# Performance work log

Hardware: AMD Instinct MI355X
Metric: run time of the kernel (lower is better)

The kernel has to match this reference:

```python
import jax, jax.numpy as jnp
import numpy as np

N, C_IN, C_OUT, H = 4096, 1024, 512, 4
D = C_OUT // H  # per-head output dim
TEMP = 1.0


def setup_inputs() -> dict:
    key = jax.random.key(0)
    ks = jax.random.split(key, 6)
    node_feats = jax.random.normal(ks[0], (N, C_IN), dtype=jnp.float32)
    # sparse 0/1 adjacency mask, avg degree ~ 0.02*N
    adj_matrix = jax.random.bernoulli(ks[1], 0.02, (N, N)).astype(jnp.float32)
    lim_w = np.sqrt(6.0 / (C_IN + D))
    lim_v = np.sqrt(6.0 / (D + 1))
    W = jax.random.uniform(ks[2], (H, C_IN, D), jnp.float32, -lim_w, lim_w)
    b = jnp.zeros((H, D), dtype=jnp.float32)
    v0 = jax.random.uniform(ks[3], (H, D), jnp.float32, -lim_v, lim_v)
    v1 = jax.random.uniform(ks[4], (H, D), jnp.float32, -lim_v, lim_v)
    return {"node_feats": node_feats, "adj_matrix": adj_matrix,
            "W": W, "b": b, "v0": v0, "v1": v1}


def reference(node_feats, adj_matrix, W, b, v0, v1):
    # per-head linear projection: [H, N, D]
    h = jnp.einsum('nc,hcd->hnd', node_feats, W) + b[:, None, :]
    f1 = jnp.einsum('hnd,hd->hn', h, v0)  # [H, N]
    f2 = jnp.einsum('hnd,hd->hn', h, v1)  # [H, N]
    logits = adj_matrix[None, :, :] * (f1[:, :, None] + f2[:, None, :])
    # torch to_sparse drops exact zeros; sparse.softmax normalizes over
    # the remaining (nonzero) entries only, zeros stay zero when densified.
    mask = logits != 0
    vals = (jax.nn.sigmoid(logits) - 0.5) / TEMP
    rowmax = jnp.max(jnp.where(mask, vals, -1e30), axis=-1, keepdims=True)
    e = jnp.where(mask, jnp.exp(vals - rowmax), 0.0)
    denom = jnp.sum(e, axis=-1, keepdims=True)
    p = jnp.where(denom > 0, e / jnp.maximum(denom, 1e-30), 0.0)
    out = jnp.einsum('hnm,hmd->hnd', p, h)  # [H, N, D]
    # concat heads along feature dim -> [N, H*D]
    return out.transpose(1, 0, 2).reshape(node_feats.shape[0], -1)
```

## Files before the change

### kernel.cpp

```cpp
#include <hip/hip_runtime.h>
#include <hip/hip_bf16.h>

#define N_NODES 4096
#define C_IN    1024
#define H_HEADS 4
#define D_HEAD  128
#define C_OUT   512
#define DEG_CAP 256

typedef __attribute__((ext_vector_type(8))) short short8;
typedef __attribute__((ext_vector_type(8))) unsigned short u16x8;
typedef __attribute__((ext_vector_type(4))) float f32x4;

__device__ __forceinline__ unsigned short f2bf(float f) {
    unsigned u = __float_as_uint(f);
    u += 0x7FFFu + ((u >> 16) & 1u);
    return (unsigned short)(u >> 16);
}
__device__ __forceinline__ float bf2f(unsigned short u) {
    return __uint_as_float((unsigned)u << 16);
}
__device__ __forceinline__ float sigv(float s) {
    return 1.f / (1.f + __expf(-s)) - 0.5f;
}

#define GLOAD_LDS16(gp, lp)                                                        \
    __builtin_amdgcn_global_load_lds(                                              \
        (const __attribute__((address_space(1))) unsigned int*)(gp),               \
        (__attribute__((address_space(3))) unsigned int*)(lp), 16, 0, 0)

__global__ void k_cvt(const float* __restrict__ X, const float* __restrict__ W,
                      unsigned short* __restrict__ Xb, unsigned short* __restrict__ Wt,
                      float* __restrict__ F12) {
    if (blockIdx.x < 2048) {
        int g = blockIdx.x * blockDim.x + threadIdx.x;
        const float4* s = (const float4*)(X + (size_t)g * 8);
        float4 a = s[0], b = s[1];
        ushort4 p0, p1;
        p0.x = f2bf(a.x); p0.y = f2bf(a.y); p0.z = f2bf(a.z); p0.w = f2bf(a.w);
        p1.x = f2bf(b.x); p1.y = f2bf(b.y); p1.z = f2bf(b.z); p1.w = f2bf(b.w);
        ushort4* d = (ushort4*)(Xb + (size_t)g * 8);
        d[0] = p0; d[1] = p1;
    } else if (blockIdx.x < 2560) {
        int g = (blockIdx.x - 2048) * blockDim.x + threadIdx.x;
        int o = g * 4;
        int c  = o & 1023;
        int hd = o >> 10;
        int d  = hd & 127;
        int h  = hd >> 7;
        const float* src = W + (size_t)h * C_IN * D_HEAD + (size_t)c * D_HEAD + d;
        ushort4 p;
        p.x = f2bf(src[0 * D_HEAD]);
        p.y = f2bf(src[1 * D_HEAD]);
        p.z = f2bf(src[2 * D_HEAD]);
        p.w = f2bf(src[3 * D_HEAD]);
        *(ushort4*)(Wt + o) = p;
    } else {
        int g = (blockIdx.x - 2560) * blockDim.x + threadIdx.x;
        *(f32x4*)(F12 + (size_t)g * 4) = (f32x4){0.f, 0.f, 0.f, 0.f};
    }
}

__global__ void k_gemm(const unsigned short* __restrict__ Xb,
                       const unsigned short* __restrict__ Wt,
                       const float* __restrict__ bias,
                       const float* __restrict__ v0, const float* __restrict__ v1,
                       unsigned short* __restrict__ Hb,
                       float* __restrict__ F1, float* __restrict__ F2) {
    __shared__ __align__(16) unsigned short ldsA[2 * 64 * 64];
    __shared__ __align__(16) unsigned short ldsB[2 * 64 * 64];
    const int t    = threadIdx.x;
    const int lane = t & 63;
    const int wid  = t >> 6;
    const int wrow = wid >> 1, wcol = wid & 1;
    const int bid  = blockIdx.x;
    const int lin  = (bid & 7) * 64 + (bid >> 3);
    const int rowStart = (lin >> 3) * 64;
    const int colStart = (lin & 7) * 64;

    f32x4 acc[2][2];
#pragma unroll
    for (int m = 0; m < 2; ++m)
#pragma unroll
        for (int n = 0; n < 2; ++n) acc[m][n] = (f32x4){0.f, 0.f, 0.f, 0.f};

    const int lrow = lane >> 2;
    const int lkq  = (lane & 3) ^ ((lane >> 3) & 3);

    auto stage = [&](int buf, int k0) {
#pragma unroll
        for (int ii = 0; ii < 2; ++ii) {
            int c  = wid * 2 + ii;
            int h  = c >> 2, rb = c & 3;
            const unsigned short* g =
                Xb + (size_t)(rowStart + rb * 16 + lrow) * C_IN + k0 + h * 32 + lkq * 8;
            GLOAD_LDS16(g, ldsA + buf * 4096 + h * 2048 + rb * 512);
        }
#pragma unroll
        for (int ii = 0; ii < 2; ++ii) {
            int c  = wid * 2 + ii;
            int h  = c >> 2, db = c & 3;
            const unsigned short* g =
                Wt + (size_t)(colStart + db * 16 + lrow) * C_IN + k0 + h * 32 + lkq * 8;
            GLOAD_LDS16(g, ldsB + buf * 4096 + h * 2048 + db * 512);
        }
    };

    stage(0, 0);
    __syncthreads();

    const int fr = lane & 15;
    const int sw = ((lane >> 4) ^ ((fr >> 1) & 3)) * 8;
    int cur = 0;
    for (int kt = 0; kt < 16; ++kt) {
        if (kt < 15) stage(cur ^ 1, (kt + 1) * 64);
        const unsigned short* __restrict__ lA = ldsA + cur * 4096;
        const unsigned short* __restrict__ lB = ldsB + cur * 4096;
#pragma unroll
        for (int h = 0; h < 2; ++h) {
            short8 bfr[2];
#pragma unroll
            for (int n = 0; n < 2; ++n)
                bfr[n] = *(const short8*)(lB + h * 2048 + (wcol * 32 + n * 16 + fr) * 32 + sw);
#pragma unroll
            for (int m = 0; m < 2; ++m) {
                short8 a = *(const short8*)(lA + h * 2048 + (wrow * 32 + m * 16 + fr) * 32 + sw);
#pragma unroll
                for (int n = 0; n < 2; ++n)
                    acc[m][n] = __builtin_amdgcn_mfma_f32_16x16x32_bf16(a, bfr[n], acc[m][n], 0, 0, 0);
            }
        }
        __syncthreads();
        cur ^= 1;
    }

    const int c0 = colStart + wcol * 32 + (lane & 15);
    const int c1 = c0 + 16;
    const int head = c0 >> 7;
    const float bb0 = bias[c0], bb1 = bias[c1];
    const float v0c0 = v0[c0], v0c1 = v0[c1];
    const float v1c0 = v1[c0], v1c1 = v1[c1];
#pragma unroll
    for (int m = 0; m < 2; ++m) {
        int row_g = rowStart + wrow * 32 + m * 16 + (lane >> 4) * 4;
#pragma unroll
        for (int r = 0; r < 4; ++r) {
            float h0 = acc[m][0][r] + bb0;
            float h1 = acc[m][1][r] + bb1;
            Hb[(size_t)(row_g + r) * C_OUT + c0] = f2bf(h0);
            Hb[(size_t)(row_g + r) * C_OUT + c1] = f2bf(h1);
            float p1 = h0 * v0c0 + h1 * v0c1;
            float p2 = h0 * v1c0 + h1 * v1c1;
#pragma unroll
            for (int off = 8; off; off >>= 1) {
                p1 += __shfl_xor(p1, off);
                p2 += __shfl_xor(p2, off);
            }
            if ((lane & 15) == 0) {
                atomicAdd(&F1[(row_g + r) * 4 + head], p1);
                atomicAdd(&F2[(row_g + r) * 4 + head], p2);
            }
        }
    }
}

__global__ void k_attn2(const float* __restrict__ adj, const unsigned short* __restrict__ Hb,
                        const float* __restrict__ F1, const float* __restrict__ F2,
                        float* __restrict__ Out) {
    __shared__ unsigned short jl[DEG_CAP];
    __shared__ float ev[DEG_CAP * 4];
    __shared__ float partial[4][C_OUT];
    __shared__ float dred[4][4];
    __shared__ int   wtot[4];

    const int i    = blockIdx.x;
    const int t    = threadIdx.x;
    const int lane = t & 63;
    const int wid  = t >> 6;
    const int headl = lane >> 4;

    const float4* arow = (const float4*)(adj + (size_t)i * N_NODES);
    float4 av[4];
#pragma unroll
    for (int r = 0; r < 4; ++r) av[r] = arow[r * 256 + t];
    float4 f1v = *(const float4*)(F1 + i * 4);

    int cnt = 0;
#pragma unroll
    for (int r = 0; r < 4; ++r)
        cnt += (av[r].x != 0.f) + (av[r].y != 0.f) + (av[r].z != 0.f) + (av[r].w != 0.f);
    int v = cnt;
#pragma unroll
    for (int off = 1; off < 64; off <<= 1) {
        int u = __shfl_up(v, off);
        if (lane >= off) v += u;
    }
    if (lane == 63) wtot[wid] = v;
    __syncthreads();
    int wpre = 0, total = 0;
#pragma unroll
    for (int w = 0; w < 4; ++w) {
        int tw = wtot[w];
        if (w < wid) wpre += tw;
        total += tw;
    }
    const int nv = min(total, DEG_CAP);
    int off = wpre + v - cnt;
#pragma unroll
    for (int r = 0; r < 4; ++r) {
        int j0 = (r * 256 + t) * 4;
        if (av[r].x != 0.f) { if (off < DEG_CAP) jl[off] = (unsigned short)j0;       off++; }
        if (av[r].y != 0.f) { if (off < DEG_CAP) jl[off] = (unsigned short)(j0 + 1); off++; }
        if (av[r].z != 0.f) { if (off < DEG_CAP) jl[off] = (unsigned short)(j0 + 2); off++; }
        if (av[r].w != 0.f) { if (off < DEG_CAP) jl[off] = (unsigned short)(j0 + 3); off++; }
    }
    __syncthreads();

    float e0 = 0.f, e1 = 0.f, e2 = 0.f, e3 = 0.f;
    if (t < nv) {
        int j = jl[t];
        float4 f2v = *(const float4*)(F2 + j * 4);
        float s0 = f1v.x + f2v.x, s1 = f1v.y + f2v.y;
        float s2 = f1v.z + f2v.z, s3 = f1v.w + f2v.w;
        e0 = (s0 != 0.f) ? __expf(sigv(s0)) : 0.f;
        e1 = (s1 != 0.f) ? __expf(sigv(s1)) : 0.f;
        e2 = (s2 != 0.f) ? __expf(sigv(s2)) : 0.f;
        e3 = (s3 != 0.f) ? __expf(sigv(s3)) : 0.f;
        ev[t * 4 + 0] = e0; ev[t * 4 + 1] = e1;
        ev[t * 4 + 2] = e2; ev[t * 4 + 3] = e3;
    }
#pragma unroll
    for (int o2 = 32; o2; o2 >>= 1) {
        e0 += __shfl_xor(e0, o2); e1 += __shfl_xor(e1, o2);
        e2 += __shfl_xor(e2, o2); e3 += __shfl_xor(e3, o2);
    }
    if (lane == 0) {
        dred[wid][0] = e0; dred[wid][1] = e1; dred[wid][2] = e2; dred[wid][3] = e3;
    }
    __syncthreads();

    float acc0[8], acc1[8];
#pragma unroll
    for (int k = 0; k < 8; ++k) { acc0[k] = 0.f; acc1[k] = 0.f; }
    const unsigned short* __restrict__ hp = Hb + lane * 8;

    int jj = wid;
#pragma unroll 4
    for (; jj + 4 < nv; jj += 8) {
        int ja = jl[jj], jb = jl[jj + 4];
        float ea = ev[jj * 4 + headl];
        float eb = ev[(jj + 4) * 4 + headl];
        u16x8 ha = *(const u16x8*)(hp + (size_t)ja * C_OUT);
        u16x8 hb = *(const u16x8*)(hp + (size_t)jb * C_OUT);
#pragma unroll
        for (int k = 0; k < 8; ++k) acc0[k] += ea * bf2f(ha[k]);
#pragma unroll
        for (int k = 0; k < 8; ++k) acc1[k] += eb * bf2f(hb[k]);
    }
    if (jj < nv) {
        int ja = jl[jj];
        float ea = ev[jj * 4 + headl];
        u16x8 ha = *(const u16x8*)(hp + (size_t)ja * C_OUT);
#pragma unroll
        for (int k = 0; k < 8; ++k) acc0[k] += ea * bf2f(ha[k]);
    }

    f32x4 lo = {acc0[0] + acc1[0], acc0[1] + acc1[1], acc0[2] + acc1[2], acc0[3] + acc1[3]};
    f32x4 hi = {acc0[4] + acc1[4], acc0[5] + acc1[5], acc0[6] + acc1[6], acc0[7] + acc1[7]};
    *(f32x4*)&partial[wid][lane * 8]     = lo;
    *(f32x4*)&partial[wid][lane * 8 + 4] = hi;
    __syncthreads();

    int head = t >> 6;
    float dn = dred[0][head] + dred[1][head] + dred[2][head] + dred[3][head];
    int c = 2 * t;
    float s0 = partial[0][c] + partial[1][c] + partial[2][c] + partial[3][c];
    float s1 = partial[0][c + 1] + partial[1][c + 1] + partial[2][c + 1] + partial[3][c + 1];
    float2 o;
    if (dn > 0.f) {
        float inv = 1.f / fmaxf(dn, 1e-30f);
        o.x = s0 * inv;
        o.y = s1 * inv;
    } else {
        o.x = 0.f; o.y = 0.f;
    }
    *(float2*)(Out + (size_t)i * C_OUT + c) = o;
}

extern "C" void kernel_launch(void* const* d_in, const int* in_sizes, int n_in,
                              void* d_out, int out_size, void* d_ws, size_t ws_size,
                              hipStream_t stream) {
    const float* X   = (const float*)d_in[0];
    const float* adj = (const float*)d_in[1];
    const float* W   = (const float*)d_in[2];
    const float* b   = (const float*)d_in[3];
    const float* v0  = (const float*)d_in[4];
    const float* v1  = (const float*)d_in[5];
    float* out = (float*)d_out;

    char* ws = (char*)d_ws;
    unsigned short* Wt  = (unsigned short*)ws;
    unsigned short* Xb  = (unsigned short*)(ws + (size_t)1 * 1024 * 1024);
    unsigned short* Hb  = (unsigned short*)(ws + (size_t)9 * 1024 * 1024);
    float*          F1  = (float*)(ws + (size_t)13 * 1024 * 1024);
    float*          F2  = F1 + N_NODES * 4;

    k_cvt<<<2592, 256, 0, stream>>>(X, W, Xb, Wt, F1);
    k_gemm<<<512, 256, 0, stream>>>(Xb, Wt, b, v0, v1, Hb, F1, F2);
    k_attn2<<<N_NODES, 256, 0, stream>>>(adj, Hb, F1, F2, out);
}
```

Measured before the change: 66.06 us.

## Overlap adjacency compaction with projection GEMM in a merged launch

Moves the dense adjacency scan and neighbor-index compaction out of the attention kernel into extra blocks of the GEMM launch, writing per-row index lists and counts to workspace. The 64MB adjacency read can then run concurrently with the MFMA projection, while the PV kernel reads only compact indices. The cost is an extra global round trip for the index lists and a merged kernel that uses 32KB of LDS for every block, including the scan blocks.

```diff
diff --git a/kernel.cpp b/kernel.cpp
--- a/kernel.cpp
+++ b/kernel.cpp
@@ -61,117 +61,160 @@
     }
 }
 
-__global__ void k_gemm(const unsigned short* __restrict__ Xb,
+__global__ void k_work(const unsigned short* __restrict__ Xb,
                        const unsigned short* __restrict__ Wt,
                        const float* __restrict__ bias,
                        const float* __restrict__ v0, const float* __restrict__ v1,
+                       const float* __restrict__ adj,
                        unsigned short* __restrict__ Hb,
-                       float* __restrict__ F1, float* __restrict__ F2) {
-    __shared__ __align__(16) unsigned short ldsA[2 * 64 * 64];
-    __shared__ __align__(16) unsigned short ldsB[2 * 64 * 64];
+                       float* __restrict__ F1, float* __restrict__ F2,
+                       unsigned short* __restrict__ idx, int* __restrict__ nnz) {
+    __shared__ __align__(16) unsigned char smem[32768];
     const int t    = threadIdx.x;
     const int lane = t & 63;
     const int wid  = t >> 6;
-    const int wrow = wid >> 1, wcol = wid & 1;
-    const int bid  = blockIdx.x;
-    const int lin  = (bid & 7) * 64 + (bid >> 3);
-    const int rowStart = (lin >> 3) * 64;
-    const int colStart = (lin & 7) * 64;
-
-    f32x4 acc[2][2];
-#pragma unroll
-    for (int m = 0; m < 2; ++m)
-#pragma unroll
-        for (int n = 0; n < 2; ++n) acc[m][n] = (f32x4){0.f, 0.f, 0.f, 0.f};
-
-    const int lrow = lane >> 2;
-    const int lkq  = (lane & 3) ^ ((lane >> 3) & 3);
-
-    auto stage = [&](int buf, int k0) {
-#pragma unroll
-        for (int ii = 0; ii < 2; ++ii) {
-            int c  = wid * 2 + ii;
-            int h  = c >> 2, rb = c & 3;
-            const unsigned short* g =
-                Xb + (size_t)(rowStart + rb * 16 + lrow) * C_IN + k0 + h * 32 + lkq * 8;
-            GLOAD_LDS16(g, ldsA + buf * 4096 + h * 2048 + rb * 512);
-        }
-#pragma unroll
-        for (int ii = 0; ii < 2; ++ii) {
-            int c  = wid * 2 + ii;
-            int h  = c >> 2, db = c & 3;
-            const unsigned short* g =
-                Wt + (size_t)(colStart + db * 16 + lrow) * C_IN + k0 + h * 32 + lkq * 8;
-            GLOAD_LDS16(g, ldsB + buf * 4096 + h * 2048 + db * 512);
-        }
-    };
-
-    stage(0, 0);
-    __syncthreads();
-
-    const int fr = lane & 15;
-    const int sw = ((lane >> 4) ^ ((fr >> 1) & 3)) * 8;
-    int cur = 0;
-    for (int kt = 0; kt < 16; ++kt) {
-        if (kt < 15) stage(cur ^ 1, (kt + 1) * 64);
-        const unsigned short* __restrict__ lA = ldsA + cur * 4096;
-        const unsigned short* __restrict__ lB = ldsB + cur * 4096;
-#pragma unroll
-        for (int h = 0; h < 2; ++h) {
-            short8 bfr[2];
-#pragma unroll
-            for (int n = 0; n < 2; ++n)
-                bfr[n] = *(const short8*)(lB + h * 2048 + (wcol * 32 + n * 16 + fr) * 32 + sw);
-#pragma unroll
-            for (int m = 0; m < 2; ++m) {
-                short8 a = *(const short8*)(lA + h * 2048 + (wrow * 32 + m * 16 + fr) * 32 + sw);
+
+    if (blockIdx.x < 512) {
+        unsigned short* ldsA = (unsigned short*)smem;
+        unsigned short* ldsB = ldsA + 2 * 64 * 64;
+        const int wrow = wid >> 1, wcol = wid & 1;
+        const int bid  = blockIdx.x;
+        const int lin  = (bid & 7) * 64 + (bid >> 3);
+        const int rowStart = (lin >> 3) * 64;
+        const int colStart = (lin & 7) * 64;
+
+        f32x4 acc[2][2];
+#pragma unroll
+        for (int m = 0; m < 2; ++m)
+#pragma unroll
+            for (int n = 0; n < 2; ++n) acc[m][n] = (f32x4){0.f, 0.f, 0.f, 0.f};
+
+        const int lrow = lane >> 2;
+        const int lkq  = (lane & 3) ^ ((lane >> 3) & 3);
+
+        auto stage = [&](int buf, int k0) {
+#pragma unroll
+            for (int ii = 0; ii < 2; ++ii) {
+                int c  = wid * 2 + ii;
+                int h  = c >> 2, rb = c & 3;
+                const unsigned short* g =
+                    Xb + (size_t)(rowStart + rb * 16 + lrow) * C_IN + k0 + h * 32 + lkq * 8;
+                GLOAD_LDS16(g, ldsA + buf * 4096 + h * 2048 + rb * 512);
+            }
+#pragma unroll
+            for (int ii = 0; ii < 2; ++ii) {
+                int c  = wid * 2 + ii;
+                int h  = c >> 2, db = c & 3;
+                const unsigned short* g =
+                    Wt + (size_t)(colStart + db * 16 + lrow) * C_IN + k0 + h * 32 + lkq * 8;
+                GLOAD_LDS16(g, ldsB + buf * 4096 + h * 2048 + db * 512);
+            }
+        };
+
+        stage(0, 0);
+        __syncthreads();
+
+        const int fr = lane & 15;
+        const int sw = ((lane >> 4) ^ ((fr >> 1) & 3)) * 8;
+        int cur = 0;
+        for (int kt = 0; kt < 16; ++kt) {
+            if (kt < 15) stage(cur ^ 1, (kt + 1) * 64);
+            const unsigned short* __restrict__ lA = ldsA + cur * 4096;
+            const unsigned short* __restrict__ lB = ldsB + cur * 4096;
+#pragma unroll
+            for (int h = 0; h < 2; ++h) {
+                short8 bfr[2];
 #pragma unroll
                 for (int n = 0; n < 2; ++n)
-                    acc[m][n] = __builtin_amdgcn_mfma_f32_16x16x32_bf16(a, bfr[n], acc[m][n], 0, 0, 0);
+                    bfr[n] = *(const short8*)(lB + h * 2048 + (wcol * 32 + n * 16 + fr) * 32 + sw);
+#pragma unroll
+                for (int m = 0; m < 2; ++m) {
+                    short8 a = *(const short8*)(lA + h * 2048 + (wrow * 32 + m * 16 + fr) * 32 + sw);
+#pragma unroll
+                    for (int n = 0; n < 2; ++n)
+                        acc[m][n] = __builtin_amdgcn_mfma_f32_16x16x32_bf16(a, bfr[n], acc[m][n], 0, 0, 0);
+                }
             }
-        }
+            __syncthreads();
+            cur ^= 1;
+        }
+
+        const int c0 = colStart + wcol * 32 + (lane & 15);
+        const int c1 = c0 + 16;
+        const int head = c0 >> 7;
+        const float bb0 = bias[c0], bb1 = bias[c1];
+        const float v0c0 = v0[c0], v0c1 = v0[c1];
+        const float v1c0 = v1[c0], v1c1 = v1[c1];
+#pragma unroll
+        for (int m = 0; m < 2; ++m) {
+            int row_g = rowStart + wrow * 32 + m * 16 + (lane >> 4) * 4;
+#pragma unroll
+            for (int r = 0; r < 4; ++r) {
+                float h0 = acc[m][0][r] + bb0;
+                float h1 = acc[m][1][r] + bb1;
+                Hb[(size_t)(row_g + r) * C_OUT + c0] = f2bf(h0);
+                Hb[(size_t)(row_g + r) * C_OUT + c1] = f2bf(h1);
+                float p1 = h0 * v0c0 + h1 * v0c1;
+                float p2 = h0 * v1c0 + h1 * v1c1;
+#pragma unroll
+                for (int off = 8; off; off >>= 1) {
+                    p1 += __shfl_xor(p1, off);
+                    p2 += __shfl_xor(p2, off);
+                }
+                if ((lane & 15) == 0) {
+                    atomicAdd(&F1[(row_g + r) * 4 + head], p1);
+                    atomicAdd(&F2[(row_g + r) * 4 + head], p2);
+                }
+            }
+        }
+    } else {
+        int* wtot = (int*)smem;
+        const int i = blockIdx.x - 512;
+        const float4* arow = (const float4*)(adj + (size_t)i * N_NODES);
+        float4 av[4];
+#pragma unroll
+        for (int r = 0; r < 4; ++r) av[r] = arow[r * 256 + t];
+
+        int cnt = 0;
+#pragma unroll
+        for (int r = 0; r < 4; ++r)
+            cnt += (av[r].x != 0.f) + (av[r].y != 0.f) + (av[r].z != 0.f) + (av[r].w != 0.f);
+        int v = cnt;
+#pragma unroll
+        for (int off = 1; off < 64; off <<= 1) {
+            int u = __shfl_up(v, off);
+            if (lane >= off) v += u;
+        }
+        if (lane == 63) wtot[wid] = v;
         __syncthreads();
-        cur ^= 1;
-    }
-
-    const int c0 = colStart + wcol * 32 + (lane & 15);
-    const int c1 = c0 + 16;
-    const int head = c0 >> 7;
-    const float bb0 = bias[c0], bb1 = bias[c1];
-    const float v0c0 = v0[c0], v0c1 = v0[c1];
-    const float v1c0 = v1[c0], v1c1 = v1[c1];
-#pragma unroll
-    for (int m = 0; m < 2; ++m) {
-        int row_g = rowStart + wrow * 32 + m * 16 + (lane >> 4) * 4;
+        int wpre = 0, total = 0;
+#pragma unroll
+        for (int w = 0; w < 4; ++w) {
+            int tw = wtot[w];
+            if (w < wid) wpre += tw;
+            total += tw;
+        }
+        int off = wpre + v - cnt;
+        unsigned short* ir = idx + (size_t)i * DEG_CAP;
 #pragma unroll
         for (int r = 0; r < 4; ++r) {
-            float h0 = acc[m][0][r] + bb0;
-            float h1 = acc[m][1][r] + bb1;
-            Hb[(size_t)(row_g + r) * C_OUT + c0] = f2bf(h0);
-            Hb[(size_t)(row_g + r) * C_OUT + c1] = f2bf(h1);
-            float p1 = h0 * v0c0 + h1 * v0c1;
-            float p2 = h0 * v1c0 + h1 * v1c1;
-#pragma unroll
-            for (int off = 8; off; off >>= 1) {
-                p1 += __shfl_xor(p1, off);
-                p2 += __shfl_xor(p2, off);
-            }
-            if ((lane & 15) == 0) {
-                atomicAdd(&F1[(row_g + r) * 4 + head], p1);
-                atomicAdd(&F2[(row_g + r) * 4 + head], p2);
-            }
-        }
-    }
-}
-
-__global__ void k_attn2(const float* __restrict__ adj, const unsigned short* __restrict__ Hb,
-                        const float* __restrict__ F1, const float* __restrict__ F2,
-                        float* __restrict__ Out) {
+            int j0 = (r * 256 + t) * 4;
+            if (av[r].x != 0.f) { if (off < DEG_CAP) ir[off] = (unsigned short)j0;       off++; }
+            if (av[r].y != 0.f) { if (off < DEG_CAP) ir[off] = (unsigned short)(j0 + 1); off++; }
+            if (av[r].z != 0.f) { if (off < DEG_CAP) ir[off] = (unsigned short)(j0 + 2); off++; }
+            if (av[r].w != 0.f) { if (off < DEG_CAP) ir[off] = (unsigned short)(j0 + 3); off++; }
+        }
+        if (t == 0) nnz[i] = min(total, DEG_CAP);
+    }
+}
+
+__global__ void k_pv(const unsigned short* __restrict__ idx, const int* __restrict__ nnz,
+                     const float* __restrict__ F1, const float* __restrict__ F2,
+                     const unsigned short* __restrict__ Hb, float* __restrict__ Out) {
     __shared__ unsigned short jl[DEG_CAP];
     __shared__ float ev[DEG_CAP * 4];
     __shared__ float partial[4][C_OUT];
     __shared__ float dred[4][4];
-    __shared__ int   wtot[4];
 
     const int i    = blockIdx.x;
     const int t    = threadIdx.x;
@@ -179,46 +222,14 @@
     const int wid  = t >> 6;
     const int headl = lane >> 4;
 
-    const float4* arow = (const float4*)(adj + (size_t)i * N_NODES);
-    float4 av[4];
-#pragma unroll
-    for (int r = 0; r < 4; ++r) av[r] = arow[r * 256 + t];
+    const int nv = nnz[i];
     float4 f1v = *(const float4*)(F1 + i * 4);
-
-    int cnt = 0;
-#pragma unroll
-    for (int r = 0; r < 4; ++r)
-        cnt += (av[r].x != 0.f) + (av[r].y != 0.f) + (av[r].z != 0.f) + (av[r].w != 0.f);
-    int v = cnt;
-#pragma unroll
-    for (int off = 1; off < 64; off <<= 1) {
-        int u = __shfl_up(v, off);
-        if (lane >= off) v += u;
-    }
-    if (lane == 63) wtot[wid] = v;
-    __syncthreads();
-    int wpre = 0, total = 0;
-#pragma unroll
-    for (int w = 0; w < 4; ++w) {
-        int tw = wtot[w];
-        if (w < wid) wpre += tw;
-        total += tw;
-    }
-    const int nv = min(total, DEG_CAP);
-    int off = wpre + v - cnt;
-#pragma unroll
-    for (int r = 0; r < 4; ++r) {
-        int j0 = (r * 256 + t) * 4;
-        if (av[r].x != 0.f) { if (off < DEG_CAP) jl[off] = (unsigned short)j0;       off++; }
-        if (av[r].y != 0.f) { if (off < DEG_CAP) jl[off] = (unsigned short)(j0 + 1); off++; }
-        if (av[r].z != 0.f) { if (off < DEG_CAP) jl[off] = (unsigned short)(j0 + 2); off++; }
-        if (av[r].w != 0.f) { if (off < DEG_CAP) jl[off] = (unsigned short)(j0 + 3); off++; }
-    }
-    __syncthreads();
+    const unsigned short* __restrict__ ji = idx + (size_t)i * DEG_CAP;
 
     float e0 = 0.f, e1 = 0.f, e2 = 0.f, e3 = 0.f;
     if (t < nv) {
-        int j = jl[t];
+        int j = ji[t];
+        jl[t] = (unsigned short)j;
         float4 f2v = *(const float4*)(F2 + j * 4);
         float s0 = f1v.x + f2v.x, s1 = f1v.y + f2v.y;
         float s2 = f1v.z + f2v.z, s3 = f1v.w + f2v.w;
@@ -304,8 +315,10 @@
     unsigned short* Hb  = (unsigned short*)(ws + (size_t)9 * 1024 * 1024);
     float*          F1  = (float*)(ws + (size_t)13 * 1024 * 1024);
     float*          F2  = F1 + N_NODES * 4;
+    unsigned short* idx = (unsigned short*)(ws + (size_t)14 * 1024 * 1024);
+    int*            nnz = (int*)(ws + (size_t)16 * 1024 * 1024);
 
     k_cvt<<<2592, 256, 0, stream>>>(X, W, Xb, Wt, F1);
-    k_gemm<<<512, 256, 0, stream>>>(Xb, Wt, b, v0, v1, Hb, F1, F2);
-    k_attn2<<<N_NODES, 256, 0, stream>>>(adj, Hb, F1, F2, out);
-}
+    k_work<<<512 + N_NODES, 256, 0, stream>>>(Xb, Wt, b, v0, v1, adj, Hb, F1, F2, idx, nnz);
+    k_pv<<<N_NODES, 256, 0, stream>>>(idx, nnz, F1, F2, Hb, out);
+}
```

Result: faster. 58.57 us (-11.3%).
